# Optimization experiments

Hardware: AMD Instinct MI355X
Metric: run time of the kernel (lower is better)

The kernel has to match this reference:

```python
import jax, jax.numpy as jnp
import numpy as np

N = 100000
E = 3200000
IN_FEAT = 128
OUT_FEAT = 128


def setup_inputs() -> dict:
    key = jax.random.key(0)
    k1, k2, k3, k4, k5, k6 = jax.random.split(key, 6)
    x = jax.random.normal(k1, (N, IN_FEAT), dtype=jnp.float32)
    edge_row = jax.random.randint(k2, (E,), 0, N, dtype=jnp.int32)
    edge_col = jax.random.randint(k3, (E,), 0, N, dtype=jnp.int32)
    edge_weight = jax.random.uniform(k4, (E,), dtype=jnp.float32)
    # nn.Linear(in_feat, out_feat) params
    bound = 1.0 / np.sqrt(IN_FEAT)
    W = jax.random.uniform(k5, (OUT_FEAT, IN_FEAT), dtype=jnp.float32, minval=-bound, maxval=bound)
    b = jax.random.uniform(k6, (OUT_FEAT,), dtype=jnp.float32, minval=-bound, maxval=bound)
    return {"x": x, "edge_row": edge_row, "edge_col": edge_col,
            "edge_weight": edge_weight, "W": W, "b": b, "k": 4}


def _spmm(edge_row, edge_col, edge_weight, x):
    # sparse adj (COO) @ dense x : gather source rows, scale, scatter-add to dest rows
    msgs = edge_weight[:, None] * x[edge_col]          # [E, F]
    return jax.ops.segment_sum(msgs, edge_row, num_segments=N)


def reference(x, edge_row, edge_col, edge_weight, W, b, k):
    for _ in range(k):
        x = _spmm(edge_row, edge_col, edge_weight, x)  # [N, F]
    # nn.Linear: x @ W^T + b
    return x @ W.T + b
```

## Files before the change

kernel.cpp:

```cpp
#include <hip/hip_runtime.h>
#include <hip/hip_fp16.h>


#define F 128
#define CH 2048
#define MAXB 256
#define RB_LOG 9
#define RB (1 << RB_LOG)
#define CAPB 18432

typedef _Float16 half8 __attribute__((ext_vector_type(8)));
typedef float f32x4 __attribute__((ext_vector_type(4)));

__global__ void prep_kernel(const float* __restrict__ W, __half* __restrict__ Wh,
                            int nw, int* __restrict__ bcnt, int nwb) {
  int blk = blockIdx.x;
  if (blk == nwb) {
    int t = threadIdx.x;
    if (t < MAXB) bcnt[t] = 0;
  } else {
    int i = blk * 256 + threadIdx.x;
    if (i < nw) Wh[i] = __float2half(W[i]);
  }
}

__global__ __launch_bounds__(256) void bucket_scatter(
    const int* __restrict__ erow, const int* __restrict__ ecol,
    const float* __restrict__ ew, int* __restrict__ bcnt,
    int2* __restrict__ mid, int e, int nb) {
  __shared__ int  rowv[CH];
  __shared__ int2 cw[CH];
  __shared__ int2 stage[CH];
  __shared__ unsigned short sbid[CH];
  __shared__ int cnt[MAXB], lstart[MAXB], gbase[MAXB], cnt2[MAXB];
  __shared__ int ps[256];
  int tid = threadIdx.x;
  int base = blockIdx.x * CH;
  int tot = e - base; if (tot > CH) tot = CH;
  for (int t = tid; t < nb; t += 256) { cnt[t] = 0; cnt2[t] = 0; }
  __syncthreads();
  for (int j = tid; j < tot; j += 256) {
    int i = base + j;
    int r = erow[i];
    rowv[j] = r;
    cw[j] = make_int2(ecol[i], __float_as_int(ew[i]));
    atomicAdd(&cnt[r >> RB_LOG], 1);
  }
  __syncthreads();
  int v = (tid < nb) ? cnt[tid] : 0;
  ps[tid] = v;
  __syncthreads();
  for (int off = 1; off < 256; off <<= 1) {
    int u = (tid >= off) ? ps[tid - off] : 0;
    __syncthreads();
    ps[tid] += u;
    __syncthreads();
  }
  if (tid < nb) lstart[tid] = ps[tid] - v;
  __syncthreads();
  for (int t = tid; t < nb; t += 256)
    if (cnt[t] > 0) gbase[t] = atomicAdd(&bcnt[t], cnt[t]);
  __syncthreads();
  for (int j = tid; j < tot; j += 256) {
    int r = rowv[j];
    int bb = r >> RB_LOG;
    int k = atomicAdd(&cnt2[bb], 1);
    int p = lstart[bb] + k;
    stage[p] = make_int2(((r & (RB - 1)) << 17) | cw[j].x, cw[j].y);
    sbid[p] = (unsigned short)bb;
  }
  __syncthreads();
  for (int j = tid; j < tot; j += 256) {
    int bb = sbid[j];
    mid[(size_t)bb * CAPB + gbase[bb] + (j - lstart[bb])] = stage[j];
  }
}

__global__ __launch_bounds__(256) void csr_sort(
    const int2* __restrict__ mid, const int* __restrict__ bcnt,
    int* __restrict__ rptr, int* __restrict__ ecols, __half* __restrict__ ewh,
    int n, int nb) {
  __shared__ int rcnt[RB];
  __shared__ int rofs[RB];
  __shared__ int psum[256];
  __shared__ int2 st[CAPB];
  int b = blockIdx.x, tid = threadIdx.x;
  int r0 = b << RB_LOG;
  int r1 = r0 + RB; if (r1 > n) r1 = n;
  int nr = r1 - r0;
  int cnt = bcnt[b];
  const int2* src = mid + (size_t)b * CAPB;

  psum[tid] = (tid < b && tid < nb) ? bcnt[tid] : 0;
  __syncthreads();
  for (int off = 128; off > 0; off >>= 1) {
    if (tid < off) psum[tid] += psum[tid + off];
    __syncthreads();
  }
  int bas = psum[0];
  __syncthreads();

  for (int r = tid; r < RB; r += 256) rcnt[r] = 0;
  __syncthreads();
  for (int i = tid; i < cnt; i += 256)
    atomicAdd(&rcnt[((unsigned)src[i].x) >> 17], 1);
  __syncthreads();
  int s2 = rcnt[2 * tid] + rcnt[2 * tid + 1];
  psum[tid] = s2;
  __syncthreads();
  for (int off = 1; off < 256; off <<= 1) {
    int u = (tid >= off) ? psum[tid - off] : 0;
    __syncthreads();
    psum[tid] += u;
    __syncthreads();
  }
  int ex = (tid > 0) ? psum[tid - 1] : 0;
  rofs[2 * tid]     = ex;
  rofs[2 * tid + 1] = ex + rcnt[2 * tid];
  __syncthreads();
  for (int r = tid; r < nr; r += 256) rptr[r0 + r] = bas + rofs[r];
  if (b == nb - 1 && tid == 0) rptr[n] = bas + cnt;
  for (int i = tid; i < cnt; i += 256) {
    int2 ed = src[i];
    int rl  = ((unsigned)ed.x) >> 17;
    int col = ed.x & 0x1FFFF;
    int p = atomicAdd(&rofs[rl], 1);
    st[p] = make_int2(col, ed.y);
  }
  __syncthreads();
  for (int i = tid; i < cnt; i += 256) {
    int2 ed = st[i];
    ecols[bas + i] = ed.x;
    ewh[bas + i]   = __float2half(__int_as_float(ed.y));
  }
}

__global__ __launch_bounds__(256) void spmm_kernel(
    const int* __restrict__ rptr, const int* __restrict__ ecols,
    const __half* __restrict__ ewh,
    const __half* __restrict__ xin, __half* __restrict__ xout, int n) {
  int lane = threadIdx.x & 63;
  int q  = lane >> 4;
  int fl = lane & 15;
  int row = (blockIdx.x << 2) + (threadIdx.x >> 6);
  if (row >= n) return;
  int s = rptr[row], e = rptr[row + 1];
  float a00 = 0.f, a01 = 0.f, a02 = 0.f, a03 = 0.f;
  float a04 = 0.f, a05 = 0.f, a06 = 0.f, a07 = 0.f;
  float b00 = 0.f, b01 = 0.f, b02 = 0.f, b03 = 0.f;
  float b04 = 0.f, b05 = 0.f, b06 = 0.f, b07 = 0.f;
  const char* xb = (const char*)xin;
  union V { int4 i4; __half2 h2[4]; };

#define UNPACK_FMA(U, W, P)                                                   \
  {                                                                           \
    float2 f0 = __half22float2((U).h2[0]);                                    \
    float2 f1 = __half22float2((U).h2[1]);                                    \
    float2 f2 = __half22float2((U).h2[2]);                                    \
    float2 f3 = __half22float2((U).h2[3]);                                    \
    P##0 = fmaf((W), f0.x, P##0); P##1 = fmaf((W), f0.y, P##1);               \
    P##2 = fmaf((W), f1.x, P##2); P##3 = fmaf((W), f1.y, P##3);               \
    P##4 = fmaf((W), f2.x, P##4); P##5 = fmaf((W), f2.y, P##5);               \
    P##6 = fmaf((W), f3.x, P##6); P##7 = fmaf((W), f3.y, P##7);               \
  }

  int i = s;
  for (; i + 7 < e; i += 8) {
    int   c0 = ecols[i + q];
    int   c1 = ecols[i + 4 + q];
    float w0 = __half2float(ewh[i + q]);
    float w1 = __half2float(ewh[i + 4 + q]);
    V v0, v1;
    v0.i4 = *(const int4*)(xb + ((size_t)(unsigned)c0 << 8) + (fl << 4));
    v1.i4 = *(const int4*)(xb + ((size_t)(unsigned)c1 << 8) + (fl << 4));
    UNPACK_FMA(v0, w0, a0);
    UNPACK_FMA(v1, w1, b0);
  }
  for (; i < e; i += 4) {
    int idx = i + q;
    bool ok = idx < e;
    int   c = ecols[ok ? idx : e - 1];
    float w = ok ? __half2float(ewh[idx]) : 0.f;
    V v;
    v.i4 = *(const int4*)(xb + ((size_t)(unsigned)c << 8) + (fl << 4));
    UNPACK_FMA(v, w, a0);
  }
#undef UNPACK_FMA

  a00 += b00; a01 += b01; a02 += b02; a03 += b03;
  a04 += b04; a05 += b05; a06 += b06; a07 += b07;
#define RED(X) X += __shfl_xor(X, 16, 64); X += __shfl_xor(X, 32, 64);
  RED(a00) RED(a01) RED(a02) RED(a03) RED(a04) RED(a05) RED(a06) RED(a07)
#undef RED
  if (q == 0) {
    union V o;
    o.h2[0] = __float22half2_rn(make_float2(a00, a01));
    o.h2[1] = __float22half2_rn(make_float2(a02, a03));
    o.h2[2] = __float22half2_rn(make_float2(a04, a05));
    o.h2[3] = __float22half2_rn(make_float2(a06, a07));
    *(int4*)((char*)xout + ((size_t)row << 8) + (fl << 4)) = o.i4;
  }
}

__global__ void f32_to_f16(const float2* __restrict__ in, __half2* __restrict__ out, int n2) {
  int i = blockIdx.x * blockDim.x + threadIdx.x;
  if (i < n2) out[i] = __float22half2_rn(in[i]);
}

__global__ __launch_bounds__(256) void linear_mfma(
    const __half* __restrict__ xin, const __half* __restrict__ Wh,
    const float* __restrict__ b, float* __restrict__ out, int n) {
  int lane = threadIdx.x & 63;
  int wv   = threadIdx.x >> 6;
  int rbase = blockIdx.x * 64 + wv * 16;
  if (rbase >= n) return;
  int arow = rbase + (lane & 15);
  if (arow >= n) arow = n - 1;
  int koff = (lane >> 4) * 8;

  half8 a0 = *(const half8*)(xin + (size_t)arow * F + 0  + koff);
  half8 a1 = *(const half8*)(xin + (size_t)arow * F + 32 + koff);
  half8 a2 = *(const half8*)(xin + (size_t)arow * F + 64 + koff);
  half8 a3 = *(const half8*)(xin + (size_t)arow * F + 96 + koff);

  int drow0 = rbase + (lane >> 4) * 4;
  int dcol  = lane & 15;
#pragma unroll
  for (int jt = 0; jt < 8; ++jt) {
    const __half* wrow = Wh + (size_t)(jt * 16 + (lane & 15)) * F + koff;
    half8 b0 = *(const half8*)(wrow + 0);
    half8 b1 = *(const half8*)(wrow + 32);
    half8 b2 = *(const half8*)(wrow + 64);
    half8 b3 = *(const half8*)(wrow + 96);
    f32x4 acc = {0.f, 0.f, 0.f, 0.f};
    acc = __builtin_amdgcn_mfma_f32_16x16x32_f16(a0, b0, acc, 0, 0, 0);
    acc = __builtin_amdgcn_mfma_f32_16x16x32_f16(a1, b1, acc, 0, 0, 0);
    acc = __builtin_amdgcn_mfma_f32_16x16x32_f16(a2, b2, acc, 0, 0, 0);
    acc = __builtin_amdgcn_mfma_f32_16x16x32_f16(a3, b3, acc, 0, 0, 0);
    float bias = b[jt * 16 + dcol];
#pragma unroll
    for (int m = 0; m < 4; ++m) {
      int r = drow0 + m;
      if (r < n) out[(size_t)r * F + jt * 16 + dcol] = acc[m] + bias;
    }
  }
}

extern "C" void kernel_launch(void* const* d_in, const int* in_sizes, int n_in,
                              void* d_out, int out_size, void* d_ws, size_t ws_size,
                              hipStream_t stream) {
  const float* x    = (const float*)d_in[0];
  const int*   erow = (const int*)d_in[1];
  const int*   ecol = (const int*)d_in[2];
  const float* ew   = (const float*)d_in[3];
  const float* W    = (const float*)d_in[4];
  const float* b    = (const float*)d_in[5];
  float* out = (float*)d_out;

  const int N = in_sizes[0] / F;
  const int E = in_sizes[1];

  char* ws = (char*)d_ws;
  size_t off = 0;
  int*    ecols = (int*)(ws + off);    off += (size_t)E * 4;
  __half* ewh   = (__half*)(ws + off); off += (size_t)E * 2;
  off = (off + 255) & ~(size_t)255;
  int*   rptr   = (int*)(ws + off);    off += (size_t)(N + 1) * 4;
  int*   bcnt   = (int*)(ws + off);    off += MAXB * 4;
  off = (off + 255) & ~(size_t)255;
  __half* Wh    = (__half*)(ws + off); off += (size_t)F * F * 2;
  off = (off + 255) & ~(size_t)255;
  __half* bufA = (__half*)(ws + off);
  __half* bufB = (__half*)(ws + off + (size_t)N * F * 2);
  int2*   mid  = (int2*)bufA;

  const int BK = 256;
  int nb = (N + RB - 1) >> RB_LOG;
  int nwb = (F * F + BK - 1) / BK;

  prep_kernel<<<nwb + 1, BK, 0, stream>>>(W, Wh, F * F, bcnt, nwb);
  bucket_scatter<<<(E + CH - 1) / CH, 256, 0, stream>>>(erow, ecol, ew, bcnt, mid, E, nb);
  csr_sort<<<nb, 256, 0, stream>>>(mid, bcnt, rptr, ecols, ewh, N, nb);

  int n2 = N * (F / 2);
  f32_to_f16<<<(n2 + BK - 1) / BK, BK, 0, stream>>>((const float2*)x, (__half2*)bufB, n2);
  int spmm_grid = (N + 3) / 4;
  spmm_kernel<<<spmm_grid, 256, 0, stream>>>(rptr, ecols, ewh, bufB, bufA, N);
  spmm_kernel<<<spmm_grid, 256, 0, stream>>>(rptr, ecols, ewh, bufA, bufB, N);
  spmm_kernel<<<spmm_grid, 256, 0, stream>>>(rptr, ecols, ewh, bufB, bufA, N);
  spmm_kernel<<<spmm_grid, 256, 0, stream>>>(rptr, ecols, ewh, bufA, bufB, N);

  linear_mfma<<<(N + 63) / 64, 256, 0, stream>>>(bufB, Wh, b, out, N);
}
```

Baseline: 561.5 us.

## Partition CSR edges by source-column phase and sweep rows in phase order

The CSR build now sorts each row's edges into 8 column-range phases and stores a per-row, per-phase pointer array. The SpMM kernel gives each wavefront 25 rows, keeps all 25 accumulators in registers, and walks the phases in the outer loop, so all waves touch roughly the same slice of x at the same time. The aim is better L2/MALL locality for the gathered rows. In exchange, each lane loads only 4 bytes per edge instead of 16, and there is less parallelism and more register pressure, which could raise latency-bound gather cost.

```diff
diff --git a/kernel.cpp b/kernel.cpp
--- a/kernel.cpp
+++ b/kernel.cpp
@@ -7,7 +7,10 @@
 #define MAXB 256
 #define RB_LOG 9
 #define RB (1 << RB_LOG)
-#define CAPB 18432
+#define CAPB 17408
+#define PH 8
+#define KEYS (RB * PH)
+#define RW 25
 
 typedef _Float16 half8 __attribute__((ext_vector_type(8)));
 typedef float f32x4 __attribute__((ext_vector_type(4)));
@@ -78,20 +81,19 @@
 
 __global__ __launch_bounds__(256) void csr_sort(
     const int2* __restrict__ mid, const int* __restrict__ bcnt,
-    int* __restrict__ rptr, int* __restrict__ ecols, __half* __restrict__ ewh,
-    int n, int nb) {
-  __shared__ int rcnt[RB];
-  __shared__ int rofs[RB];
+    int* __restrict__ rptr8, int* __restrict__ ecols, __half* __restrict__ ewh,
+    int n, int nb, unsigned minv8) {
+  __shared__ int cnt[KEYS];
   __shared__ int psum[256];
   __shared__ int2 st[CAPB];
   int b = blockIdx.x, tid = threadIdx.x;
   int r0 = b << RB_LOG;
   int r1 = r0 + RB; if (r1 > n) r1 = n;
   int nr = r1 - r0;
-  int cnt = bcnt[b];
+  int cntE = bcnt[b];
   const int2* src = mid + (size_t)b * CAPB;
 
-  psum[tid] = (tid < b && tid < nb) ? bcnt[tid] : 0;
+  psum[tid] = (tid < b) ? bcnt[tid] : 0;
   __syncthreads();
   for (int off = 128; off > 0; off >>= 1) {
     if (tid < off) psum[tid] += psum[tid + off];
@@ -100,105 +102,102 @@
   int bas = psum[0];
   __syncthreads();
 
-  for (int r = tid; r < RB; r += 256) rcnt[r] = 0;
-  __syncthreads();
-  for (int i = tid; i < cnt; i += 256)
-    atomicAdd(&rcnt[((unsigned)src[i].x) >> 17], 1);
-  __syncthreads();
-  int s2 = rcnt[2 * tid] + rcnt[2 * tid + 1];
-  psum[tid] = s2;
-  __syncthreads();
-  for (int off = 1; off < 256; off <<= 1) {
-    int u = (tid >= off) ? psum[tid - off] : 0;
-    __syncthreads();
-    psum[tid] += u;
-    __syncthreads();
-  }
-  int ex = (tid > 0) ? psum[tid - 1] : 0;
-  rofs[2 * tid]     = ex;
-  rofs[2 * tid + 1] = ex + rcnt[2 * tid];
-  __syncthreads();
-  for (int r = tid; r < nr; r += 256) rptr[r0 + r] = bas + rofs[r];
-  if (b == nb - 1 && tid == 0) rptr[n] = bas + cnt;
-  for (int i = tid; i < cnt; i += 256) {
+  for (int t = tid; t < KEYS; t += 256) cnt[t] = 0;
+  __syncthreads();
+  for (int i = tid; i < cntE; i += 256) {
     int2 ed = src[i];
     int rl  = ((unsigned)ed.x) >> 17;
     int col = ed.x & 0x1FFFF;
-    int p = atomicAdd(&rofs[rl], 1);
-    st[p] = make_int2(col, ed.y);
-  }
-  __syncthreads();
-  for (int i = tid; i < cnt; i += 256) {
+    unsigned ph = __umulhi((unsigned)col, minv8);
+    if (ph > PH - 1) ph = PH - 1;
+    atomicAdd(&cnt[(rl << 3) | ph], 1);
+  }
+  __syncthreads();
+  int v[16]; int sum = 0;
+#pragma unroll
+  for (int t = 0; t < 16; ++t) { v[t] = cnt[tid * 16 + t]; sum += v[t]; }
+  psum[tid] = sum;
+  __syncthreads();
+  for (int off = 1; off < 256; off <<= 1) {
+    int u = (tid >= off) ? psum[tid - off] : 0;
+    __syncthreads();
+    psum[tid] += u;
+    __syncthreads();
+  }
+  int run = (tid > 0) ? psum[tid - 1] : 0;
+#pragma unroll
+  for (int t = 0; t < 16; ++t) { cnt[tid * 16 + t] = run; run += v[t]; }
+  __syncthreads();
+  for (int t = tid; t < nr * PH; t += 256) rptr8[(r0 << 3) + t] = bas + cnt[t];
+  if (b == nb - 1 && tid == 0) rptr8[(size_t)n << 3] = bas + cntE;
+  for (int i = tid; i < cntE; i += 256) {
+    int2 ed = src[i];
+    int rl  = ((unsigned)ed.x) >> 17;
+    int col = ed.x & 0x1FFFF;
+    unsigned ph = __umulhi((unsigned)col, minv8);
+    if (ph > PH - 1) ph = PH - 1;
+    int p = atomicAdd(&cnt[(rl << 3) | ph], 1);
+    st[p] = make_int2(col << 8, ed.y);
+  }
+  __syncthreads();
+  for (int i = tid; i < cntE; i += 256) {
     int2 ed = st[i];
     ecols[bas + i] = ed.x;
     ewh[bas + i]   = __float2half(__int_as_float(ed.y));
   }
 }
 
-__global__ __launch_bounds__(256) void spmm_kernel(
-    const int* __restrict__ rptr, const int* __restrict__ ecols,
-    const __half* __restrict__ ewh,
-    const __half* __restrict__ xin, __half* __restrict__ xout, int n) {
+__global__ __launch_bounds__(256, 4) void spmm_persist(
+    const int* __restrict__ rptr8, const int* __restrict__ ecols,
+    const __half* __restrict__ ewh, const __half* __restrict__ xin,
+    __half* __restrict__ xout, int n) {
   int lane = threadIdx.x & 63;
-  int q  = lane >> 4;
-  int fl = lane & 15;
-  int row = (blockIdx.x << 2) + (threadIdx.x >> 6);
-  if (row >= n) return;
-  int s = rptr[row], e = rptr[row + 1];
-  float a00 = 0.f, a01 = 0.f, a02 = 0.f, a03 = 0.f;
-  float a04 = 0.f, a05 = 0.f, a06 = 0.f, a07 = 0.f;
-  float b00 = 0.f, b01 = 0.f, b02 = 0.f, b03 = 0.f;
-  float b04 = 0.f, b05 = 0.f, b06 = 0.f, b07 = 0.f;
+  int g = (blockIdx.x << 2) + (threadIdx.x >> 6);
+  int r0 = g * RW;
   const char* xb = (const char*)xin;
-  union V { int4 i4; __half2 h2[4]; };
-
-#define UNPACK_FMA(U, W, P)                                                   \
-  {                                                                           \
-    float2 f0 = __half22float2((U).h2[0]);                                    \
-    float2 f1 = __half22float2((U).h2[1]);                                    \
-    float2 f2 = __half22float2((U).h2[2]);                                    \
-    float2 f3 = __half22float2((U).h2[3]);                                    \
-    P##0 = fmaf((W), f0.x, P##0); P##1 = fmaf((W), f0.y, P##1);               \
-    P##2 = fmaf((W), f1.x, P##2); P##3 = fmaf((W), f1.y, P##3);               \
-    P##4 = fmaf((W), f2.x, P##4); P##5 = fmaf((W), f2.y, P##5);               \
-    P##6 = fmaf((W), f3.x, P##6); P##7 = fmaf((W), f3.y, P##7);               \
-  }
-
-  int i = s;
-  for (; i + 7 < e; i += 8) {
-    int   c0 = ecols[i + q];
-    int   c1 = ecols[i + 4 + q];
-    float w0 = __half2float(ewh[i + q]);
-    float w1 = __half2float(ewh[i + 4 + q]);
-    V v0, v1;
-    v0.i4 = *(const int4*)(xb + ((size_t)(unsigned)c0 << 8) + (fl << 4));
-    v1.i4 = *(const int4*)(xb + ((size_t)(unsigned)c1 << 8) + (fl << 4));
-    UNPACK_FMA(v0, w0, a0);
-    UNPACK_FMA(v1, w1, b0);
-  }
-  for (; i < e; i += 4) {
-    int idx = i + q;
-    bool ok = idx < e;
-    int   c = ecols[ok ? idx : e - 1];
-    float w = ok ? __half2float(ewh[idx]) : 0.f;
-    V v;
-    v.i4 = *(const int4*)(xb + ((size_t)(unsigned)c << 8) + (fl << 4));
-    UNPACK_FMA(v, w, a0);
-  }
-#undef UNPACK_FMA
-
-  a00 += b00; a01 += b01; a02 += b02; a03 += b03;
-  a04 += b04; a05 += b05; a06 += b06; a07 += b07;
-#define RED(X) X += __shfl_xor(X, 16, 64); X += __shfl_xor(X, 32, 64);
-  RED(a00) RED(a01) RED(a02) RED(a03) RED(a04) RED(a05) RED(a06) RED(a07)
-#undef RED
-  if (q == 0) {
-    union V o;
-    o.h2[0] = __float22half2_rn(make_float2(a00, a01));
-    o.h2[1] = __float22half2_rn(make_float2(a02, a03));
-    o.h2[2] = __float22half2_rn(make_float2(a04, a05));
-    o.h2[3] = __float22half2_rn(make_float2(a06, a07));
-    *(int4*)((char*)xout + ((size_t)row << 8) + (fl << 4)) = o.i4;
+  float2 acc[RW];
+#pragma unroll
+  for (int j = 0; j < RW; ++j) acc[j] = make_float2(0.f, 0.f);
+
+  for (int s = 0; s < PH; ++s) {
+#pragma unroll
+    for (int j = 0; j < RW; ++j) {
+      int r = r0 + j;
+      if (r < n) {
+        int e0 = rptr8[(r << 3) + s];
+        int e1 = rptr8[(r << 3) + s + 1];
+        float ax = acc[j].x, ay = acc[j].y;
+        int e = e0;
+        for (; e + 1 < e1; e += 2) {
+          int c0 = ecols[e], c1 = ecols[e + 1];
+          float w0 = __half2float(ewh[e]);
+          float w1 = __half2float(ewh[e + 1]);
+          union { int i; __half2 h2; } u0, u1;
+          u0.i = *(const int*)(xb + (size_t)(unsigned)c0 + (lane << 2));
+          u1.i = *(const int*)(xb + (size_t)(unsigned)c1 + (lane << 2));
+          float2 f0 = __half22float2(u0.h2);
+          float2 f1 = __half22float2(u1.h2);
+          ax = fmaf(w0, f0.x, ax); ay = fmaf(w0, f0.y, ay);
+          ax = fmaf(w1, f1.x, ax); ay = fmaf(w1, f1.y, ay);
+        }
+        if (e < e1) {
+          int c0 = ecols[e];
+          float w0 = __half2float(ewh[e]);
+          union { int i; __half2 h2; } u0;
+          u0.i = *(const int*)(xb + (size_t)(unsigned)c0 + (lane << 2));
+          float2 f0 = __half22float2(u0.h2);
+          ax = fmaf(w0, f0.x, ax); ay = fmaf(w0, f0.y, ay);
+        }
+        acc[j].x = ax; acc[j].y = ay;
+      }
+    }
+  }
+#pragma unroll
+  for (int j = 0; j < RW; ++j) {
+    int r = r0 + j;
+    if (r < n)
+      *(__half2*)((char*)xout + ((size_t)r << 8) + (lane << 2)) =
+          __float22half2_rn(acc[j]);
   }
 }
 
@@ -265,7 +264,7 @@
   int*    ecols = (int*)(ws + off);    off += (size_t)E * 4;
   __half* ewh   = (__half*)(ws + off); off += (size_t)E * 2;
   off = (off + 255) & ~(size_t)255;
-  int*   rptr   = (int*)(ws + off);    off += (size_t)(N + 1) * 4;
+  int*   rptr8  = (int*)(ws + off);    off += ((size_t)N * PH + 1) * 4;
   int*   bcnt   = (int*)(ws + off);    off += MAXB * 4;
   off = (off + 255) & ~(size_t)255;
   __half* Wh    = (__half*)(ws + off); off += (size_t)F * F * 2;
@@ -277,18 +276,19 @@
   const int BK = 256;
   int nb = (N + RB - 1) >> RB_LOG;
   int nwb = (F * F + BK - 1) / BK;
+  unsigned minv8 = (unsigned)(((unsigned long long)PH << 32) / (unsigned)N + 1);
 
   prep_kernel<<<nwb + 1, BK, 0, stream>>>(W, Wh, F * F, bcnt, nwb);
   bucket_scatter<<<(E + CH - 1) / CH, 256, 0, stream>>>(erow, ecol, ew, bcnt, mid, E, nb);
-  csr_sort<<<nb, 256, 0, stream>>>(mid, bcnt, rptr, ecols, ewh, N, nb);
+  csr_sort<<<nb, 256, 0, stream>>>(mid, bcnt, rptr8, ecols, ewh, N, nb, minv8);
 
   int n2 = N * (F / 2);
   f32_to_f16<<<(n2 + BK - 1) / BK, BK, 0, stream>>>((const float2*)x, (__half2*)bufB, n2);
-  int spmm_grid = (N + 3) / 4;
-  spmm_kernel<<<spmm_grid, 256, 0, stream>>>(rptr, ecols, ewh, bufB, bufA, N);
-  spmm_kernel<<<spmm_grid, 256, 0, stream>>>(rptr, ecols, ewh, bufA, bufB, N);
-  spmm_kernel<<<spmm_grid, 256, 0, stream>>>(rptr, ecols, ewh, bufB, bufA, N);
-  spmm_kernel<<<spmm_grid, 256, 0, stream>>>(rptr, ecols, ewh, bufA, bufB, N);
+  int pgrid = (N + 4 * RW - 1) / (4 * RW);
+  spmm_persist<<<pgrid, 256, 0, stream>>>(rptr8, ecols, ewh, bufB, bufA, N);
+  spmm_persist<<<pgrid, 256, 0, stream>>>(rptr8, ecols, ewh, bufA, bufB, N);
+  spmm_persist<<<pgrid, 256, 0, stream>>>(rptr8, ecols, ewh, bufB, bufA, N);
+  spmm_persist<<<pgrid, 256, 0, stream>>>(rptr8, ecols, ewh, bufA, bufB, N);
 
   linear_mfma<<<(N + 63) / 64, 256, 0, stream>>>(bufB, Wh, b, out, N);
 }
```

After: 1.513 ms. 169% more time.
